# Kernel tuning notes

Measured on AMD Instinct MI355X. Metric: run time of the kernel, lower is better.

The kernel has to match this reference:

```python
import jax, jax.numpy as jnp
import numpy as np

P = 8          # patch_num_in == patch_num_out
R = 16         # patch_resolution (pixels per patch side)
C = 2          # dim_channel
D = 512        # dim_token
NH = 8         # nhead
DFF = 2048     # dim_feedforward
L = 6          # num_layers
PAIRS = 5      # demo_num
BS = 8
HW = P * R     # 128
S = PAIRS * 2 * P * P  # 640 tokens
EPS = 1e-5


def _patchify(x):
    # x: (N, c, H, W) -> (N, P*P, c*R*R)
    N, c, H, W = x.shape
    x = x.reshape(N, c, P, R, P, R).transpose(0, 2, 4, 1, 3, 5)
    return x.reshape(N, P * P, c * R * R)


def _depatchify(x, c):
    # x: (N, P*P, c*R*R) -> (N, c, P*R, P*R)
    N = x.shape[0]
    x = x.reshape(N, P, P, c, R, R).transpose(0, 3, 1, 4, 2, 5)
    return x.reshape(N, c, P * R, P * R)


def _ln(x, s, b):
    mu = jnp.mean(x, axis=-1, keepdims=True)
    var = jnp.mean(jnp.square(x - mu), axis=-1, keepdims=True)
    return (x - mu) * jax.lax.rsqrt(var + EPS) * s + b


def _block_lowtri_additive_mask(seq_len):
    blk = jnp.arange(seq_len) // (P * P)  # alternating init/end blocks of size P*P
    allowed = blk[:, None] >= blk[None, :]
    return jnp.where(allowed, 0.0, -jnp.inf).astype(jnp.float32)


def setup_inputs() -> dict:
    key = jax.random.key(0)
    ks = jax.random.split(key, 20)
    s = 0.02
    f32 = jnp.float32
    inp = {
        "init": jax.random.normal(ks[0], (BS, PAIRS, C, HW, HW), f32),
        "end": jax.random.normal(ks[1], (BS, PAIRS, C, HW, HW), f32),
        "c_mask": jnp.ones((BS, C), dtype=bool),
        "pre_W": (jax.random.normal(ks[2], (D, C * R * R), f32) * s),
        "pre_b": jnp.zeros((D,), f32),
        "post_W": (jax.random.normal(ks[3], (C * R * R, D), f32) * s),
        "post_b": jnp.zeros((C * R * R,), f32),
        "patch_pos": jax.random.normal(ks[4], (P * P, D), f32),
        "func_pos": jax.random.normal(ks[5], (PAIRS * 2, D), f32),
        "Wqkv": (jax.random.normal(ks[6], (L, 3 * D, D), f32) * s),
        "bqkv": jnp.zeros((L, 3 * D), f32),
        "Wo": (jax.random.normal(ks[7], (L, D, D), f32) * s),
        "bo": jnp.zeros((L, D), f32),
        "ln1_s": jnp.ones((L, D), f32),
        "ln1_b": jnp.zeros((L, D), f32),
        "ln2_s": jnp.ones((L, D), f32),
        "ln2_b": jnp.zeros((L, D), f32),
        "W1": (jax.random.normal(ks[8], (L, DFF, D), f32) * s),
        "b1": jnp.zeros((L, DFF), f32),
        "W2": (jax.random.normal(ks[9], (L, D, DFF), f32) * s),
        "b2": jnp.zeros((L, D), f32),
    }
    return inp


def _forward(init, end, pre_W, pre_b, post_W, post_b, patch_pos, func_pos,
             Wqkv, bqkv, Wo, bo, ln1_s, ln1_b, ln2_s, ln2_b, W1, b1, W2, b2):
    bs, pairs = init.shape[0], init.shape[1]
    # interleave (init, end) per pair: (bs, pairs, 2, c, h, w)
    x = jnp.concatenate([init[:, :, None], end[:, :, None]], axis=2)
    f = x.reshape(-1, C, HW, HW)
    f = _patchify(f)                                    # (N, P*P, C*R*R)
    f = f @ pre_W.T + pre_b                             # (N, P*P, D)
    f = f + patch_pos                                   # patch pos encoding
    f = f.reshape(bs, pairs * 2, P * P, D)
    f = f + func_pos[: pairs * 2][None, :, None, :]     # func pos encoding
    seq = pairs * 2 * P * P
    f = f.reshape(bs, seq, D)

    amask = _block_lowtri_additive_mask(seq)            # (S, S) additive
    dh = D // NH
    scale = 1.0 / np.sqrt(dh).astype(np.float32)

    for l in range(L):
        qkv = f @ Wqkv[l].T + bqkv[l]                   # (bs, S, 3D)
        q, k, v = jnp.split(qkv, 3, axis=-1)
        q = q.reshape(bs, seq, NH, dh).transpose(0, 2, 1, 3)
        k = k.reshape(bs, seq, NH, dh).transpose(0, 2, 1, 3)
        v = v.reshape(bs, seq, NH, dh).transpose(0, 2, 1, 3)
        scores = jnp.einsum('bhqd,bhkd->bhqk', q, k) * scale + amask
        attn = jax.nn.softmax(scores, axis=-1)
        o = jnp.einsum('bhqk,bhkd->bhqd', attn, v)
        o = o.transpose(0, 2, 1, 3).reshape(bs, seq, D)
        o = o @ Wo[l].T + bo[l]
        f = _ln(f + o, ln1_s[l], ln1_b[l])              # post-norm (PyTorch default)
        ff = jax.nn.gelu(f @ W1[l].T + b1[l], approximate=False) @ W2[l].T + b2[l]
        f = _ln(f + ff, ln2_s[l], ln2_b[l])

    f = f.reshape(bs, pairs, 2, P * P, D)[:, :, 0]      # read prediction off init slots
    f = f @ post_W.T + post_b                           # (bs, pairs, P*P, C*R*R)
    f = f.reshape(bs * pairs, P * P, C * R * R)
    f = _depatchify(f, C)
    return f.reshape(bs, pairs, C, HW, HW)


def reference(init, end, c_mask, pre_W, pre_b, post_W, post_b, patch_pos, func_pos,
              Wqkv, bqkv, Wo, bo, ln1_s, ln1_b, ln2_s, ln2_b, W1, b1, W2, b2):
    # c_mask is unpacked but unused by the original forward
    return _forward(init, end, pre_W, pre_b, post_W, post_b, patch_pos, func_pos,
                    Wqkv, bqkv, Wo, bo, ln1_s, ln1_b, ln2_s, ln2_b, W1, b1, W2, b2)
```

## Files before the change

### kernel.cpp

```cpp
#include <hip/hip_runtime.h>
#include <hip/hip_bf16.h>

#define BSZ 8
#define PAIRS 5
#define NCH 2
#define HWP 128
#define PP 64
#define DIM 512
#define NHEAD 8
#define DHEAD 64
#define DFF 2048
#define NLAYER 6
#define SEQ 640
#define NTOK (BSZ * SEQ)
#define FIN 10
#define MPOST (BSZ * PAIRS * PP)

typedef unsigned short u16;
typedef __bf16 bf16_t;
typedef __attribute__((ext_vector_type(8))) __bf16 bf16x8;
typedef __attribute__((ext_vector_type(4))) float f32x4;
#define MFMA16(a, b, c) __builtin_amdgcn_mfma_f32_16x16x32_bf16(a, b, c, 0, 0, 0)

__device__ __forceinline__ u16 f2b(float x) {
  unsigned u = __float_as_uint(x);
  return (u16)((u + 0x7fffu + ((u >> 16) & 1u)) >> 16);
}

__device__ __forceinline__ float gelu_t(float x) {
  float y = 0.7978845608f * (x + 0.044715f * x * x * x);
  y = fminf(fmaxf(y, -10.f), 10.f);
  float e = __expf(2.f * y);
  return 0.5f * x * (1.f + (e - 1.f) / (e + 1.f));
}

__device__ __forceinline__ void dma16(const u16* g, void* l) {
  __builtin_amdgcn_global_load_lds(
      (const __attribute__((address_space(1))) void*)g,
      (__attribute__((address_space(3))) void*)l, 16, 0, 0);
}

__global__ __launch_bounds__(256) void k_cvt2(const float* __restrict__ a,
                                              const float* __restrict__ b,
                                              u16* __restrict__ da,
                                              u16* __restrict__ db, int n) {
  int i = blockIdx.x * 256 + threadIdx.x;
  if (i < n) { da[i] = f2b(a[i]); db[i] = f2b(b[i]); }
}

#define W_QKV (3 * DIM * DIM)
#define W_O (DIM * DIM)
#define W_1 (DFF * DIM)
#define OFF_O W_QKV
#define OFF_1 (W_QKV + W_O)
#define OFF_2 (W_QKV + W_O + W_1)
#define W_ALL (W_QKV + W_O + 2 * W_1)
__global__ __launch_bounds__(256) void k_cvtw(const float* __restrict__ wq,
                                              const float* __restrict__ wo,
                                              const float* __restrict__ w1,
                                              const float* __restrict__ w2,
                                              u16* __restrict__ dst) {
  int i = blockIdx.x * 256 + threadIdx.x;
  const float* src;
  int off;
  if (i < OFF_O) { src = wq; off = i; }
  else if (i < OFF_1) { src = wo; off = i - OFF_O; }
  else if (i < OFF_2) { src = w1; off = i - OFF_1; }
  else { src = w2; off = i - OFF_2; }
  dst[i] = f2b(src[off]);
}

__global__ __launch_bounds__(256) void k_patchify(const float* __restrict__ init,
                                                  const float* __restrict__ endp,
                                                  u16* __restrict__ A) {
  int i = blockIdx.x * 256 + threadIdx.x;
  int d = i & 511;
  int g = i >> 9;
  int p = g & 63;
  int fi = (g >> 6) % FIN;
  int b = g / SEQ;
  int e = fi & 1;
  int pr = fi >> 1;
  int c = d >> 8;
  int r1 = (d >> 4) & 15;
  int r2 = d & 15;
  int row = ((p >> 3) << 4) + r1;
  int col = ((p & 7) << 4) + r2;
  const float* src = e ? endp : init;
  size_t off = ((size_t)((b * PAIRS + pr) * NCH + c) << 14) + (size_t)row * HWP + col;
  A[i] = f2b(src[off]);
}

__global__ __launch_bounds__(256) void k_addpos(const float* __restrict__ pin, int KS,
                                                float* __restrict__ f,
                                                u16* __restrict__ fb,
                                                const float* __restrict__ pre_b,
                                                const float* __restrict__ patch_pos,
                                                const float* __restrict__ func_pos) {
  int i = blockIdx.x * 256 + threadIdx.x;
  int d = i & 511;
  int g = i >> 9;
  int p = g & 63;
  int fi = (g >> 6) % FIN;
  float v = pre_b[d] + patch_pos[p * DIM + d] + func_pos[fi * DIM + d];
  for (int z = 0; z < KS; ++z) v += pin[(size_t)z * NTOK * DIM + i];
  f[i] = v;
  fb[i] = f2b(v);
}

template <int NT>
__global__ __launch_bounds__(256) void k_mma(const u16* __restrict__ A,
                                             const u16* __restrict__ B,
                                             const float* __restrict__ bias,
                                             u16* __restrict__ outB,
                                             float* __restrict__ outP,
                                             int M, int N, int K, int Kblk, int act) {
  constexpr int FJ = NT / 32;
  constexpr int NC4 = (4 + NT / 16) / 4;
  __shared__ __align__(16) bf16_t As[2][64][32];
  __shared__ __align__(16) bf16_t Bs[2][NT][32];
  const int t = threadIdx.x;
  const int w = t >> 6, lane = t & 63, quad = lane >> 4, l16 = lane & 15;
  int bx = blockIdx.x, by = blockIdx.y;
  if ((gridDim.y & 7) == 0) {
    int lin = bx + gridDim.x * by;
    int YT = gridDim.y >> 3;
    int xcd = lin & 7, slot = lin >> 3;
    by = xcd * YT + slot % YT;
    bx = slot / YT;
  }
  const int row0 = by << 6, col0 = bx * NT;
  const size_t kOff = (size_t)blockIdx.z * Kblk;
  const int mB = (w & 1) << 5;
  const int nB = (w >> 1) * (NT / 2);
  const u16* ApL = A + (size_t)(row0 + (lane >> 2)) * K + kOff + ((lane & 3) << 3);
  const u16* BpL = B + (size_t)(col0 + (lane >> 2)) * K + kOff + ((lane & 3) << 3);

  f32x4 acc[2][FJ];
#pragma unroll
  for (int i = 0; i < 2; ++i)
#pragma unroll
    for (int j = 0; j < FJ; ++j) acc[i][j] = (f32x4){0.f, 0.f, 0.f, 0.f};

  auto stage = [&](int bu, int kk) {
#pragma unroll
    for (int s = 0; s < NC4; ++s) {
      int c = NC4 * w + s;
      if (c < 4) dma16(ApL + (size_t)(c * 16) * K + kk, &As[bu][c * 16][0]);
      else dma16(BpL + (size_t)((c - 4) * 16) * K + kk, &Bs[bu][(c - 4) * 16][0]);
    }
  };

  const int iters = Kblk >> 5;
  stage(0, 0);
  for (int it = 0; it < iters; ++it) {
    const int cur = it & 1;
    __syncthreads();
    if (it + 1 < iters) stage(cur ^ 1, (it + 1) << 5);
    bf16x8 af[2], bfr[FJ];
#pragma unroll
    for (int i = 0; i < 2; ++i)
      af[i] = *(const bf16x8*)&As[cur][mB + i * 16 + l16][quad * 8];
#pragma unroll
    for (int j = 0; j < FJ; ++j)
      bfr[j] = *(const bf16x8*)&Bs[cur][nB + j * 16 + l16][quad * 8];
#pragma unroll
    for (int i = 0; i < 2; ++i)
#pragma unroll
      for (int j = 0; j < FJ; ++j) acc[i][j] = MFMA16(af[i], bfr[j], acc[i][j]);
  }

  if (outB) {
#pragma unroll
    for (int i = 0; i < 2; ++i)
#pragma unroll
      for (int reg = 0; reg < 4; ++reg) {
        int m = row0 + mB + i * 16 + quad * 4 + reg;
#pragma unroll
        for (int j = 0; j < FJ; ++j) {
          int n = col0 + nB + j * 16 + l16;
          float v = acc[i][j][reg] + bias[n];
          if (act) v = gelu_t(v);
          outB[(size_t)m * N + n] = f2b(v);
        }
      }
  } else {
    float* dst = outP + (size_t)blockIdx.z * M * N;
#pragma unroll
    for (int i = 0; i < 2; ++i)
#pragma unroll
      for (int reg = 0; reg < 4; ++reg) {
        int m = row0 + mB + i * 16 + quad * 4 + reg;
#pragma unroll
        for (int j = 0; j < FJ; ++j) {
          int n = col0 + nB + j * 16 + l16;
          dst[(size_t)m * N + n] = acc[i][j][reg];
        }
      }
  }
}

__global__ __launch_bounds__(256) void k_attn(const u16* __restrict__ qkv,
                                              u16* __restrict__ o) {
  __shared__ bf16_t Qs[64][72];
  __shared__ bf16_t Ks[64][72];
  __shared__ bf16_t Vs[64][72];
  __shared__ bf16_t Ps[64][72];
  const int t = threadIdx.x;
  const int w = t >> 6, lane = t & 63, quad = lane >> 4, l16 = lane & 15;
  const int qblk = blockIdx.x, h = blockIdx.y, b = blockIdx.z;
  const int q0 = qblk << 6;
  const u16* base = qkv + (size_t)b * SEQ * (3 * DIM);
  const int sr = t >> 2;
  const int sd = (t & 3) << 4;
  {
    const u16* qp = base + (size_t)(q0 + sr) * (3 * DIM) + h * DHEAD + sd;
    *(bf16x8*)&Qs[sr][sd] = *(const bf16x8*)(const void*)qp;
    *(bf16x8*)&Qs[sr][sd + 8] = *(const bf16x8*)(const void*)(qp + 8);
  }
  __syncthreads();
  bf16x8 aQ0 = *(const bf16x8*)&Qs[w * 16 + l16][quad * 8];
  bf16x8 aQ1 = *(const bf16x8*)&Qs[w * 16 + l16][32 + quad * 8];
  f32x4 accO[4];
#pragma unroll
  for (int j = 0; j < 4; ++j) accO[j] = (f32x4){0.f, 0.f, 0.f, 0.f};
  float mSt[4] = {-1e30f, -1e30f, -1e30f, -1e30f};
  float lSt[4] = {0.f, 0.f, 0.f, 0.f};
  const int ntile = qblk + 1;
  for (int kt = 0; kt < ntile; ++kt) {
    {
      const u16* kp = base + (size_t)(kt * 64 + sr) * (3 * DIM) + DIM + h * DHEAD + sd;
      *(bf16x8*)&Ks[sr][sd] = *(const bf16x8*)(const void*)kp;
      *(bf16x8*)&Ks[sr][sd + 8] = *(const bf16x8*)(const void*)(kp + 8);
      const u16* vp = base + (size_t)(kt * 64 + sr) * (3 * DIM) + 2 * DIM + h * DHEAD + sd;
      bf16x8 v0 = *(const bf16x8*)(const void*)vp;
      bf16x8 v1 = *(const bf16x8*)(const void*)(vp + 8);
#pragma unroll
      for (int e = 0; e < 8; ++e) Vs[sd + e][sr] = v0[e];
#pragma unroll
      for (int e = 0; e < 8; ++e) Vs[sd + 8 + e][sr] = v1[e];
    }
    __syncthreads();
    f32x4 s[4];
#pragma unroll
    for (int j = 0; j < 4; ++j) {
      bf16x8 b0 = *(const bf16x8*)&Ks[j * 16 + l16][quad * 8];
      bf16x8 b1 = *(const bf16x8*)&Ks[j * 16 + l16][32 + quad * 8];
      s[j] = (f32x4){0.f, 0.f, 0.f, 0.f};
      s[j] = MFMA16(aQ0, b0, s[j]);
      s[j] = MFMA16(aQ1, b1, s[j]);
      s[j] *= 0.125f;
    }
#pragma unroll
    for (int reg = 0; reg < 4; ++reg) {
      float mx = fmaxf(fmaxf(s[0][reg], s[1][reg]), fmaxf(s[2][reg], s[3][reg]));
      mx = fmaxf(mx, __shfl_xor(mx, 1));
      mx = fmaxf(mx, __shfl_xor(mx, 2));
      mx = fmaxf(mx, __shfl_xor(mx, 4));
      mx = fmaxf(mx, __shfl_xor(mx, 8));
      float mNew = fmaxf(mSt[reg], mx);
      float alpha = __expf(mSt[reg] - mNew);
      mSt[reg] = mNew;
      float rs = 0.f;
#pragma unroll
      for (int j = 0; j < 4; ++j) {
        float p = __expf(s[j][reg] - mNew);
        s[j][reg] = p;
        rs += p;
      }
      rs += __shfl_xor(rs, 1);
      rs += __shfl_xor(rs, 2);
      rs += __shfl_xor(rs, 4);
      rs += __shfl_xor(rs, 8);
      lSt[reg] = lSt[reg] * alpha + rs;
#pragma unroll
      for (int j = 0; j < 4; ++j) accO[j][reg] *= alpha;
    }
#pragma unroll
    for (int j = 0; j < 4; ++j)
#pragma unroll
      for (int reg = 0; reg < 4; ++reg)
        *(u16*)&Ps[w * 16 + quad * 4 + reg][j * 16 + l16] = f2b(s[j][reg]);
    __syncthreads();
    bf16x8 aP0 = *(const bf16x8*)&Ps[w * 16 + l16][quad * 8];
    bf16x8 aP1 = *(const bf16x8*)&Ps[w * 16 + l16][32 + quad * 8];
#pragma unroll
    for (int jd = 0; jd < 4; ++jd) {
      bf16x8 b0 = *(const bf16x8*)&Vs[jd * 16 + l16][quad * 8];
      bf16x8 b1 = *(const bf16x8*)&Vs[jd * 16 + l16][32 + quad * 8];
      accO[jd] = MFMA16(aP0, b0, accO[jd]);
      accO[jd] = MFMA16(aP1, b1, accO[jd]);
    }
    __syncthreads();
  }
#pragma unroll
  for (int reg = 0; reg < 4; ++reg) {
    float inv = 1.0f / lSt[reg];
    int row = q0 + w * 16 + quad * 4 + reg;
#pragma unroll
    for (int jd = 0; jd < 4; ++jd)
      o[((size_t)(b * SEQ + row)) * DIM + h * DHEAD + jd * 16 + l16] =
          f2b(accO[jd][reg] * inv);
  }
}

__global__ __launch_bounds__(256) void k_red_ln(const float* __restrict__ part, int KS,
                                                const float* __restrict__ bias,
                                                float* __restrict__ f,
                                                u16* __restrict__ fb,
                                                const float* __restrict__ s,
                                                const float* __restrict__ bvec) {
  const int row = blockIdx.x;
  const int t = threadIdx.x;
  const size_t base = (size_t)row * DIM;
  float x0 = f[base + t] + bias[t];
  float x1 = f[base + t + 256] + bias[t + 256];
  for (int z = 0; z < KS; ++z) {
    x0 += part[(size_t)z * NTOK * DIM + base + t];
    x1 += part[(size_t)z * NTOK * DIM + base + t + 256];
  }
  float sum = x0 + x1;
  float sq = x0 * x0 + x1 * x1;
#pragma unroll
  for (int off = 32; off; off >>= 1) {
    sum += __shfl_xor(sum, off);
    sq += __shfl_xor(sq, off);
  }
  __shared__ float rs[4], rq[4];
  const int w = t >> 6, lane = t & 63;
  if (lane == 0) { rs[w] = sum; rq[w] = sq; }
  __syncthreads();
  float tot = rs[0] + rs[1] + rs[2] + rs[3];
  float tq2 = rq[0] + rq[1] + rq[2] + rq[3];
  float mu = tot * (1.0f / 512.0f);
  float var = tq2 * (1.0f / 512.0f) - mu * mu;
  float rstd = rsqrtf(var + 1e-5f);
  float v0 = (x0 - mu) * rstd * s[t] + bvec[t];
  float v1 = (x1 - mu) * rstd * s[t + 256] + bvec[t + 256];
  f[base + t] = v0;
  f[base + t + 256] = v1;
  fb[base + t] = f2b(v0);
  fb[base + t + 256] = f2b(v1);
}

__global__ __launch_bounds__(256) void k_gather(const u16* __restrict__ fb,
                                                u16* __restrict__ Ap) {
  int i = blockIdx.x * 256 + threadIdx.x;
  int m = i >> 9, d = i & 511;
  int p = m & 63, pr = (m >> 6) % PAIRS, b = m / (PAIRS * PP);
  int g = b * SEQ + pr * 128 + p;
  Ap[i] = fb[(size_t)g * DIM + d];
}

__global__ __launch_bounds__(256) void k_scatter(const float* __restrict__ part, int KS,
                                                 const float* __restrict__ bias,
                                                 float* __restrict__ out) {
  int i = blockIdx.x * 256 + threadIdx.x;
  int m = i >> 9, n = i & 511;
  float v = bias[n];
  for (int z = 0; z < KS; ++z) v += part[(size_t)z * MPOST * DIM + i];
  int p = m & 63, pr = (m >> 6) % PAIRS, b = m / (PAIRS * PP);
  int c = n >> 8, r1 = (n >> 4) & 15, r2 = n & 15;
  int row = ((p >> 3) << 4) + r1, col = ((p & 7) << 4) + r2;
  size_t off = ((size_t)((b * PAIRS + pr) * NCH + c) << 14) + (size_t)row * HWP + col;
  out[off] = v;
}

extern "C" void kernel_launch(void* const* d_in, const int* in_sizes, int n_in,
                              void* d_out, int out_size, void* d_ws, size_t ws_size,
                              hipStream_t stream) {
  const float* init = (const float*)d_in[0];
  const float* endp = (const float*)d_in[1];
  const float* pre_W = (const float*)d_in[3];
  const float* pre_b = (const float*)d_in[4];
  const float* post_W = (const float*)d_in[5];
  const float* post_b = (const float*)d_in[6];
  const float* patch_pos = (const float*)d_in[7];
  const float* func_pos = (const float*)d_in[8];
  const float* Wqkv = (const float*)d_in[9];
  const float* bqkv = (const float*)d_in[10];
  const float* Wo = (const float*)d_in[11];
  const float* bo = (const float*)d_in[12];
  const float* ln1_s = (const float*)d_in[13];
  const float* ln1_b = (const float*)d_in[14];
  const float* ln2_s = (const float*)d_in[15];
  const float* ln2_b = (const float*)d_in[16];
  const float* W1 = (const float*)d_in[17];
  const float* b1 = (const float*)d_in[18];
  const float* W2 = (const float*)d_in[19];
  const float* b2 = (const float*)d_in[20];
  float* out = (float*)d_out;

  char* p = (char*)d_ws;
  float* buf_f = (float*)p;    p += (size_t)NTOK * DIM * 4;
  u16* buf_fb = (u16*)p;       p += (size_t)NTOK * DIM * 2;
  u16* buf_attn = (u16*)p;     p += (size_t)NTOK * DIM * 2;
  u16* shared_b = (u16*)p;     p += (size_t)NTOK * DFF * 2;
  u16* wB = (u16*)p;           p += (size_t)W_ALL * 2;
  u16* wPre = (u16*)p;         p += (size_t)DIM * DIM * 2;
  u16* wPost = (u16*)p;        p += (size_t)DIM * DIM * 2;
  float* partial = (float*)p;
  u16* buf_patch = shared_b;
  u16* buf_qkv = shared_b;
  u16* buf_hid = shared_b;
  u16* buf_apost = shared_b;

  dim3 blk(256);
  const int elems = NTOK * DIM;

  k_cvt2<<<(DIM * DIM + 255) / 256, blk, 0, stream>>>(pre_W, post_W, wPre, wPost,
                                                      DIM * DIM);
  k_patchify<<<elems / 256, blk, 0, stream>>>(init, endp, buf_patch);
  k_mma<64><<<dim3(8, 80, 2), blk, 0, stream>>>(
      buf_patch, wPre, nullptr, nullptr, partial, NTOK, DIM, DIM, DIM / 2, 0);
  k_addpos<<<elems / 256, blk, 0, stream>>>(partial, 2, buf_f, buf_fb, pre_b,
                                            patch_pos, func_pos);

  for (int l = 0; l < NLAYER; ++l) {
    k_cvtw<<<W_ALL / 256, blk, 0, stream>>>(
        Wqkv + (size_t)l * W_QKV, Wo + (size_t)l * W_O, W1 + (size_t)l * W_1,
        W2 + (size_t)l * W_1, wB);
    k_mma<128><<<dim3(12, 80, 1), blk, 0, stream>>>(
        buf_fb, wB, bqkv + (size_t)l * 3 * DIM, buf_qkv, nullptr,
        NTOK, 3 * DIM, DIM, DIM, 0);
    k_attn<<<dim3(SEQ / 64, NHEAD, BSZ), blk, 0, stream>>>(buf_qkv, buf_attn);
    k_mma<64><<<dim3(8, 80, 2), blk, 0, stream>>>(
        buf_attn, wB + OFF_O, nullptr, nullptr, partial, NTOK, DIM, DIM, DIM / 2, 0);
    k_red_ln<<<NTOK, blk, 0, stream>>>(partial, 2, bo + (size_t)l * DIM, buf_f,
                                       buf_fb, ln1_s + (size_t)l * DIM,
                                       ln1_b + (size_t)l * DIM);
    k_mma<128><<<dim3(16, 80, 1), blk, 0, stream>>>(
        buf_fb, wB + OFF_1, b1 + (size_t)l * DFF, buf_hid, nullptr,
        NTOK, DFF, DIM, DIM, 1);
    k_mma<64><<<dim3(8, 80, 2), blk, 0, stream>>>(
        buf_hid, wB + OFF_2, nullptr, nullptr, partial, NTOK, DIM, DFF, DFF / 2, 0);
    k_red_ln<<<NTOK, blk, 0, stream>>>(partial, 2, b2 + (size_t)l * DIM, buf_f,
                                       buf_fb, ln2_s + (size_t)l * DIM,
                                       ln2_b + (size_t)l * DIM);
  }

  k_gather<<<(MPOST * DIM) / 256, blk, 0, stream>>>(buf_fb, buf_apost);
  k_mma<64><<<dim3(8, 40, 2), blk, 0, stream>>>(
      buf_apost, wPost, nullptr, nullptr, partial, MPOST, DIM, DIM, DIM / 2, 0);
  k_scatter<<<(MPOST * DIM) / 256, blk, 0, stream>>>(partial, 2, post_b, out);
}
```

Baseline: 1.007 ms.

## Fuse weight conversion, pre/post GEMM epilogues, and relax GEMM barriers

Converts all layers' weights to bf16 in one up-front kernel instead of once per layer. Folds the positional-add into the pre-projection GEMM epilogue, and folds the gather and scatter into the post-projection GEMM's row addressing and epilogue. Drops split-K for the K=512 GEMMs, which removes a partial-sum pass. Replaces __syncthreads with explicit vmcnt waits and s_barrier so the next stage's DMA can overlap the current stage's loads. This cuts launches and intermediate traffic, but uses a larger weight buffer and relies on correct manual waitcnt counts.

```diff
diff --git a/kernel.cpp b/kernel.cpp
--- a/kernel.cpp
+++ b/kernel.cpp
@@ -40,14 +40,6 @@
       (__attribute__((address_space(3))) void*)l, 16, 0, 0);
 }
 
-__global__ __launch_bounds__(256) void k_cvt2(const float* __restrict__ a,
-                                              const float* __restrict__ b,
-                                              u16* __restrict__ da,
-                                              u16* __restrict__ db, int n) {
-  int i = blockIdx.x * 256 + threadIdx.x;
-  if (i < n) { da[i] = f2b(a[i]); db[i] = f2b(b[i]); }
-}
-
 #define W_QKV (3 * DIM * DIM)
 #define W_O (DIM * DIM)
 #define W_1 (DFF * DIM)
@@ -55,19 +47,30 @@
 #define OFF_1 (W_QKV + W_O)
 #define OFF_2 (W_QKV + W_O + W_1)
 #define W_ALL (W_QKV + W_O + 2 * W_1)
-__global__ __launch_bounds__(256) void k_cvtw(const float* __restrict__ wq,
-                                              const float* __restrict__ wo,
-                                              const float* __restrict__ w1,
-                                              const float* __restrict__ w2,
-                                              u16* __restrict__ dst) {
+#define PREPOST (2 * DIM * DIM)
+#define N_CVT (PREPOST + NLAYER * W_ALL)
+
+__global__ __launch_bounds__(256) void k_cvt_all(const float* __restrict__ preW,
+                                                 const float* __restrict__ postW,
+                                                 const float* __restrict__ wq,
+                                                 const float* __restrict__ wo,
+                                                 const float* __restrict__ w1,
+                                                 const float* __restrict__ w2,
+                                                 u16* __restrict__ dst) {
   int i = blockIdx.x * 256 + threadIdx.x;
-  const float* src;
-  int off;
-  if (i < OFF_O) { src = wq; off = i; }
-  else if (i < OFF_1) { src = wo; off = i - OFF_O; }
-  else if (i < OFF_2) { src = w1; off = i - OFF_1; }
-  else { src = w2; off = i - OFF_2; }
-  dst[i] = f2b(src[off]);
+  float v;
+  if (i < DIM * DIM) v = preW[i];
+  else if (i < PREPOST) v = postW[i - DIM * DIM];
+  else {
+    int j = i - PREPOST;
+    int l = j / W_ALL;
+    int r = j - l * W_ALL;
+    if (r < OFF_O) v = wq[(size_t)l * W_QKV + r];
+    else if (r < OFF_1) v = wo[(size_t)l * W_O + r - OFF_O];
+    else if (r < OFF_2) v = w1[(size_t)l * W_1 + r - OFF_1];
+    else v = w2[(size_t)l * W_1 + r - OFF_2];
+  }
+  dst[i] = f2b(v);
 }
 
 __global__ __launch_bounds__(256) void k_patchify(const float* __restrict__ init,
@@ -91,32 +94,18 @@
   A[i] = f2b(src[off]);
 }
 
-__global__ __launch_bounds__(256) void k_addpos(const float* __restrict__ pin, int KS,
-                                                float* __restrict__ f,
-                                                u16* __restrict__ fb,
-                                                const float* __restrict__ pre_b,
-                                                const float* __restrict__ patch_pos,
-                                                const float* __restrict__ func_pos) {
-  int i = blockIdx.x * 256 + threadIdx.x;
-  int d = i & 511;
-  int g = i >> 9;
-  int p = g & 63;
-  int fi = (g >> 6) % FIN;
-  float v = pre_b[d] + patch_pos[p * DIM + d] + func_pos[fi * DIM + d];
-  for (int z = 0; z < KS; ++z) v += pin[(size_t)z * NTOK * DIM + i];
-  f[i] = v;
-  fb[i] = f2b(v);
-}
-
-template <int NT>
+template <int NT, int MODE>
 __global__ __launch_bounds__(256) void k_mma(const u16* __restrict__ A,
                                              const u16* __restrict__ B,
                                              const float* __restrict__ bias,
                                              u16* __restrict__ outB,
                                              float* __restrict__ outP,
+                                             float* __restrict__ outF,
+                                             const float* __restrict__ pp,
+                                             const float* __restrict__ fp,
                                              int M, int N, int K, int Kblk, int act) {
   constexpr int FJ = NT / 32;
-  constexpr int NC4 = (4 + NT / 16) / 4;
+  constexpr int NC = (4 + NT / 16) / 4;
   __shared__ __align__(16) bf16_t As[2][64][32];
   __shared__ __align__(16) bf16_t Bs[2][NT][32];
   const int t = threadIdx.x;
@@ -133,8 +122,19 @@
   const size_t kOff = (size_t)blockIdx.z * Kblk;
   const int mB = (w & 1) << 5;
   const int nB = (w >> 1) * (NT / 2);
-  const u16* ApL = A + (size_t)(row0 + (lane >> 2)) * K + kOff + ((lane & 3) << 3);
-  const u16* BpL = B + (size_t)(col0 + (lane >> 2)) * K + kOff + ((lane & 3) << 3);
+
+  const u16* aP[4];
+#pragma unroll
+  for (int c = 0; c < 4; ++c) {
+    int r = row0 + c * 16 + (lane >> 2);
+    int g = r;
+    if (MODE == 3) {
+      int p = r & 63, pr = (r >> 6) % PAIRS, b = r / (PAIRS * PP);
+      g = b * SEQ + pr * 128 + p;
+    }
+    aP[c] = A + (size_t)g * K + kOff + ((lane & 3) << 3);
+  }
+  const u16* bP = B + (size_t)(col0 + (lane >> 2)) * K + kOff + ((lane & 3) << 3);
 
   f32x4 acc[2][FJ];
 #pragma unroll
@@ -144,10 +144,10 @@
 
   auto stage = [&](int bu, int kk) {
 #pragma unroll
-    for (int s = 0; s < NC4; ++s) {
-      int c = NC4 * w + s;
-      if (c < 4) dma16(ApL + (size_t)(c * 16) * K + kk, &As[bu][c * 16][0]);
-      else dma16(BpL + (size_t)((c - 4) * 16) * K + kk, &Bs[bu][(c - 4) * 16][0]);
+    for (int s = 0; s < NC; ++s) {
+      int c = NC * w + s;
+      if (c < 4) dma16(aP[c] + kk, &As[bu][c * 16][0]);
+      else dma16(bP + (size_t)((c - 4) * 16) * K + kk, &Bs[bu][(c - 4) * 16][0]);
     }
   };
 
@@ -155,8 +155,16 @@
   stage(0, 0);
   for (int it = 0; it < iters; ++it) {
     const int cur = it & 1;
-    __syncthreads();
-    if (it + 1 < iters) stage(cur ^ 1, (it + 1) << 5);
+    if (it > 0) asm volatile("s_barrier" ::: "memory");
+    const bool more = (it + 1 < iters);
+    if (more) stage(cur ^ 1, (it + 1) << 5);
+    if (more) {
+      if (NC == 3) asm volatile("s_waitcnt vmcnt(3)" ::: "memory");
+      else asm volatile("s_waitcnt vmcnt(2)" ::: "memory");
+    } else {
+      asm volatile("s_waitcnt vmcnt(0)" ::: "memory");
+    }
+    asm volatile("s_barrier" ::: "memory");
     bf16x8 af[2], bfr[FJ];
 #pragma unroll
     for (int i = 0; i < 2; ++i)
@@ -170,34 +178,37 @@
       for (int j = 0; j < FJ; ++j) acc[i][j] = MFMA16(af[i], bfr[j], acc[i][j]);
   }
 
-  if (outB) {
-#pragma unroll
-    for (int i = 0; i < 2; ++i)
-#pragma unroll
-      for (int reg = 0; reg < 4; ++reg) {
-        int m = row0 + mB + i * 16 + quad * 4 + reg;
-#pragma unroll
-        for (int j = 0; j < FJ; ++j) {
-          int n = col0 + nB + j * 16 + l16;
-          float v = acc[i][j][reg] + bias[n];
+#pragma unroll
+  for (int i = 0; i < 2; ++i)
+#pragma unroll
+    for (int reg = 0; reg < 4; ++reg) {
+      int m = row0 + mB + i * 16 + quad * 4 + reg;
+#pragma unroll
+      for (int j = 0; j < FJ; ++j) {
+        int n = col0 + nB + j * 16 + l16;
+        float v = acc[i][j][reg];
+        if (MODE == 0) {
+          v += bias[n];
           if (act) v = gelu_t(v);
           outB[(size_t)m * N + n] = f2b(v);
+        } else if (MODE == 1) {
+          outP[(size_t)blockIdx.z * M * N + (size_t)m * N + n] = v;
+        } else if (MODE == 2) {
+          int p = m & 63, fi = (m >> 6) % FIN;
+          v += bias[n] + pp[p * DIM + n] + fp[fi * DIM + n];
+          outF[(size_t)m * N + n] = v;
+          outB[(size_t)m * N + n] = f2b(v);
+        } else {
+          v += bias[n];
+          int p = m & 63, pr = (m >> 6) % PAIRS, b = m / (PAIRS * PP);
+          int c = n >> 8, r1 = (n >> 4) & 15, r2 = n & 15;
+          int row = ((p >> 3) << 4) + r1, col = ((p & 7) << 4) + r2;
+          size_t off = ((size_t)((b * PAIRS + pr) * NCH + c) << 14) +
+                       (size_t)row * HWP + col;
+          outF[off] = v;
         }
       }
-  } else {
-    float* dst = outP + (size_t)blockIdx.z * M * N;
-#pragma unroll
-    for (int i = 0; i < 2; ++i)
-#pragma unroll
-      for (int reg = 0; reg < 4; ++reg) {
-        int m = row0 + mB + i * 16 + quad * 4 + reg;
-#pragma unroll
-        for (int j = 0; j < FJ; ++j) {
-          int n = col0 + nB + j * 16 + l16;
-          dst[(size_t)m * N + n] = acc[i][j][reg];
-        }
-      }
-  }
+    }
 }
 
 __global__ __launch_bounds__(256) void k_attn(const u16* __restrict__ qkv,
@@ -341,29 +352,6 @@
   f[base + t + 256] = v1;
   fb[base + t] = f2b(v0);
   fb[base + t + 256] = f2b(v1);
-}
-
-__global__ __launch_bounds__(256) void k_gather(const u16* __restrict__ fb,
-                                                u16* __restrict__ Ap) {
-  int i = blockIdx.x * 256 + threadIdx.x;
-  int m = i >> 9, d = i & 511;
-  int p = m & 63, pr = (m >> 6) % PAIRS, b = m / (PAIRS * PP);
-  int g = b * SEQ + pr * 128 + p;
-  Ap[i] = fb[(size_t)g * DIM + d];
-}
-
-__global__ __launch_bounds__(256) void k_scatter(const float* __restrict__ part, int KS,
-                                                 const float* __restrict__ bias,
-                                                 float* __restrict__ out) {
-  int i = blockIdx.x * 256 + threadIdx.x;
-  int m = i >> 9, n = i & 511;
-  float v = bias[n];
-  for (int z = 0; z < KS; ++z) v += part[(size_t)z * MPOST * DIM + i];
-  int p = m & 63, pr = (m >> 6) % PAIRS, b = m / (PAIRS * PP);
-  int c = n >> 8, r1 = (n >> 4) & 15, r2 = n & 15;
-  int row = ((p >> 3) << 4) + r1, col = ((p & 7) << 4) + r2;
-  size_t off = ((size_t)((b * PAIRS + pr) * NCH + c) << 14) + (size_t)row * HWP + col;
-  out[off] = v;
 }
 
 extern "C" void kernel_launch(void* const* d_in, const int* in_sizes, int n_in,
@@ -396,51 +384,48 @@
   u16* buf_fb = (u16*)p;       p += (size_t)NTOK * DIM * 2;
   u16* buf_attn = (u16*)p;     p += (size_t)NTOK * DIM * 2;
   u16* shared_b = (u16*)p;     p += (size_t)NTOK * DFF * 2;
-  u16* wB = (u16*)p;           p += (size_t)W_ALL * 2;
-  u16* wPre = (u16*)p;         p += (size_t)DIM * DIM * 2;
-  u16* wPost = (u16*)p;        p += (size_t)DIM * DIM * 2;
+  u16* wAll = (u16*)p;         p += (size_t)N_CVT * 2;
   float* partial = (float*)p;
   u16* buf_patch = shared_b;
   u16* buf_qkv = shared_b;
   u16* buf_hid = shared_b;
-  u16* buf_apost = shared_b;
+  u16* wPre = wAll;
+  u16* wPost = wAll + DIM * DIM;
+  u16* wL = wAll + PREPOST;
 
   dim3 blk(256);
   const int elems = NTOK * DIM;
 
-  k_cvt2<<<(DIM * DIM + 255) / 256, blk, 0, stream>>>(pre_W, post_W, wPre, wPost,
-                                                      DIM * DIM);
+  k_cvt_all<<<N_CVT / 256, blk, 0, stream>>>(pre_W, post_W, Wqkv, Wo, W1, W2, wAll);
   k_patchify<<<elems / 256, blk, 0, stream>>>(init, endp, buf_patch);
-  k_mma<64><<<dim3(8, 80, 2), blk, 0, stream>>>(
-      buf_patch, wPre, nullptr, nullptr, partial, NTOK, DIM, DIM, DIM / 2, 0);
-  k_addpos<<<elems / 256, blk, 0, stream>>>(partial, 2, buf_f, buf_fb, pre_b,
-                                            patch_pos, func_pos);
+  k_mma<64, 2><<<dim3(8, 80, 1), blk, 0, stream>>>(
+      buf_patch, wPre, pre_b, buf_fb, nullptr, buf_f, patch_pos, func_pos,
+      NTOK, DIM, DIM, DIM, 0);
 
   for (int l = 0; l < NLAYER; ++l) {
-    k_cvtw<<<W_ALL / 256, blk, 0, stream>>>(
-        Wqkv + (size_t)l * W_QKV, Wo + (size_t)l * W_O, W1 + (size_t)l * W_1,
-        W2 + (size_t)l * W_1, wB);
-    k_mma<128><<<dim3(12, 80, 1), blk, 0, stream>>>(
-        buf_fb, wB, bqkv + (size_t)l * 3 * DIM, buf_qkv, nullptr,
-        NTOK, 3 * DIM, DIM, DIM, 0);
+    u16* wB = wL + (size_t)l * W_ALL;
+    k_mma<128, 0><<<dim3(12, 80, 1), blk, 0, stream>>>(
+        buf_fb, wB, bqkv + (size_t)l * 3 * DIM, buf_qkv, nullptr, nullptr, nullptr,
+        nullptr, NTOK, 3 * DIM, DIM, DIM, 0);
     k_attn<<<dim3(SEQ / 64, NHEAD, BSZ), blk, 0, stream>>>(buf_qkv, buf_attn);
-    k_mma<64><<<dim3(8, 80, 2), blk, 0, stream>>>(
-        buf_attn, wB + OFF_O, nullptr, nullptr, partial, NTOK, DIM, DIM, DIM / 2, 0);
-    k_red_ln<<<NTOK, blk, 0, stream>>>(partial, 2, bo + (size_t)l * DIM, buf_f,
+    k_mma<64, 1><<<dim3(8, 80, 1), blk, 0, stream>>>(
+        buf_attn, wB + OFF_O, nullptr, nullptr, partial, nullptr, nullptr, nullptr,
+        NTOK, DIM, DIM, DIM, 0);
+    k_red_ln<<<NTOK, blk, 0, stream>>>(partial, 1, bo + (size_t)l * DIM, buf_f,
                                        buf_fb, ln1_s + (size_t)l * DIM,
                                        ln1_b + (size_t)l * DIM);
-    k_mma<128><<<dim3(16, 80, 1), blk, 0, stream>>>(
-        buf_fb, wB + OFF_1, b1 + (size_t)l * DFF, buf_hid, nullptr,
-        NTOK, DFF, DIM, DIM, 1);
-    k_mma<64><<<dim3(8, 80, 2), blk, 0, stream>>>(
-        buf_hid, wB + OFF_2, nullptr, nullptr, partial, NTOK, DIM, DFF, DFF / 2, 0);
+    k_mma<128, 0><<<dim3(16, 80, 1), blk, 0, stream>>>(
+        buf_fb, wB + OFF_1, b1 + (size_t)l * DFF, buf_hid, nullptr, nullptr, nullptr,
+        nullptr, NTOK, DFF, DIM, DIM, 1);
+    k_mma<64, 1><<<dim3(8, 80, 2), blk, 0, stream>>>(
+        buf_hid, wB + OFF_2, nullptr, nullptr, partial, nullptr, nullptr, nullptr,
+        NTOK, DIM, DFF, DFF / 2, 0);
     k_red_ln<<<NTOK, blk, 0, stream>>>(partial, 2, b2 + (size_t)l * DIM, buf_f,
                                        buf_fb, ln2_s + (size_t)l * DIM,
                                        ln2_b + (size_t)l * DIM);
   }
 
-  k_gather<<<(MPOST * DIM) / 256, blk, 0, stream>>>(buf_fb, buf_apost);
-  k_mma<64><<<dim3(8, 40, 2), blk, 0, stream>>>(
-      buf_apost, wPost, nullptr, nullptr, partial, MPOST, DIM, DIM, DIM / 2, 0);
-  k_scatter<<<(MPOST * DIM) / 256, blk, 0, stream>>>(partial, 2, post_b, out);
-}
+  k_mma<64, 3><<<dim3(8, 40, 1), blk, 0, stream>>>(
+      buf_fb, wPost, post_b, nullptr, nullptr, out, nullptr, nullptr,
+      MPOST, DIM, DIM, DIM, 0);
+}
```

New measurement: 972.6 us. -3.4%, faster.
